# Performance work log

Measured on AMD Instinct MI355X. Metric: run time of the kernel, lower is better.

Reference implementation:

```python
import jax, jax.numpy as jnp
import numpy as np

IN_DIM, OUT_DIM, K, NUM = 512, 512, 3, 16
BATCH = 256


def setup_inputs() -> dict:
    key = jax.random.key(0)
    k1, k2 = jax.random.split(key, 2)
    x = jax.random.normal(k1, (BATCH, IN_DIM), dtype=jnp.float32)
    # uniform grid on [-1,1] extended by K knots each side (extend_grid)
    h = 2.0 / NUM
    g1d = jnp.arange(-K, NUM + K + 1, dtype=jnp.float32) * h - 1.0  # (NUM+1+2K,)
    grid = jnp.tile(g1d[None, :], (IN_DIM, 1))  # (in_dim, 24)
    coef = jax.random.normal(k2, (IN_DIM, OUT_DIM, NUM + K), dtype=jnp.float32) * 0.1
    scale_sp = jnp.ones((IN_DIM, OUT_DIM), jnp.float32) * (1.0 / np.sqrt(IN_DIM).astype(np.float32))
    mask = jnp.ones((IN_DIM, OUT_DIM), jnp.float32)
    return {"x": x, "grid": grid, "coef": coef, "scale_sp": scale_sp, "mask": mask}


def b_spline_basis(x, grid, k):
    # x: (B, I); grid: (I, G).  Cox-de Boor recursion, vectorized.
    xg = x[:, :, None]          # (B, I, 1)
    g = grid[None, :, :]        # (1, I, G)
    B = ((xg >= g[:, :, :-1]) & (xg < g[:, :, 1:])).astype(x.dtype)  # order-0
    for kk in range(1, k + 1):
        B = ((xg - g[:, :, :-(kk + 1)]) / (g[:, :, kk:-1] - g[:, :, :-(kk + 1)]) * B[:, :, :-1]
             + (g[:, :, kk + 1:] - xg) / (g[:, :, kk + 1:] - g[:, :, 1:-kk]) * B[:, :, 1:])
    return B  # (B, I, NUM + K)


def reference(x, grid, coef, scale_sp, mask):
    base = jax.nn.silu(x)                              # (B, I) base_fun branch
    Bmat = b_spline_basis(x, grid, K)                  # (B, I, NUM+K)
    y = jnp.einsum('big,iog->bio', Bmat, coef)         # coef2curve -> (B, I, O)
    y = (base[:, :, None] + scale_sp[None, :, :] * y) * mask[None, :, :]
    return jnp.sum(y, axis=1)                          # (B, O)
```

## Files before the change

### kernel.cpp

```cpp
#include <hip/hip_runtime.h>

#define IN_DIM   512
#define OUT_DIM  512
#define KDEG     3
#define BATCH    256
#define NB       19
#define NG       23
#define KAUG     20
#define KTOT     (IN_DIM * KAUG)

typedef short  bf16x8 __attribute__((ext_vector_type(8)));
typedef float  f32x4  __attribute__((ext_vector_type(4)));

__device__ __forceinline__ unsigned short f2bf(float f) {
    union { float f; unsigned int u; } v; v.f = f;
    unsigned int r = (v.u + 0x7FFF + ((v.u >> 16) & 1)) >> 16;
    return (unsigned short)r;
}

__global__ void build_A(const float* __restrict__ X,
                        const float* __restrict__ G,
                        unsigned short* __restrict__ A) {
    int t = blockIdx.x * blockDim.x + threadIdx.x;
    if (t >= BATCH * IN_DIM) return;
    int b = t / IN_DIM;
    int i = t - b * IN_DIM;

    float x = X[t];

    float gr[NG];
    const float* g = G + i * NG;
#pragma unroll
    for (int j = 0; j < NG; j++) gr[j] = g[j];

    float B[NG - 1];
#pragma unroll
    for (int j = 0; j < NG - 1; j++)
        B[j] = (x >= gr[j] && x < gr[j + 1]) ? 1.0f : 0.0f;

#pragma unroll
    for (int kk = 1; kk <= KDEG; kk++) {
#pragma unroll
        for (int j = 0; j < NG - 1 - kk; j++) {
            float d1 = gr[j + kk] - gr[j];
            float d2 = gr[j + kk + 1] - gr[j + 1];
            B[j] = (x - gr[j]) / d1 * B[j] +
                   (gr[j + kk + 1] - x) / d2 * B[j + 1];
        }
    }

    unsigned short v[KAUG];
#pragma unroll
    for (int j = 0; j < NB; j++) v[j] = f2bf(B[j]);
    v[NB] = f2bf(x / (1.0f + __expf(-x)));

    unsigned int* dst = (unsigned int*)(A + (size_t)b * KTOT + i * KAUG);
    const unsigned int* src = (const unsigned int*)v;
#pragma unroll
    for (int d = 0; d < KAUG / 2; d++) dst[d] = src[d];
}

#define BN     32
#define SPLITS 32
#define ICH    16
#define KCH    (ICH * KAUG)
#define LDS_K  (KCH + 8)

__global__ __launch_bounds__(512, 4) void gemm_fused(
        const unsigned short* __restrict__ A,
        const float* __restrict__ coef,
        const float* __restrict__ scale_sp,
        const float* __restrict__ mask,
        float* __restrict__ P) {
    __shared__ __align__(16) unsigned short Bs[BN * LDS_K];

    int tid = threadIdx.x;
    int o0 = blockIdx.x * BN;
    int i0 = blockIdx.z * ICH;
    int kbase = blockIdx.z * KCH;

    {
        int o  = tid & 31;
        int di = tid >> 5;
        int io = (i0 + di) * OUT_DIM + (o0 + o);
        float m  = mask[io];
        float sm = scale_sp[io] * m;
        const float* c = coef + (size_t)io * NB;

        __align__(8) unsigned short v[KAUG];
#pragma unroll
        for (int g = 0; g < NB; g++) v[g] = f2bf(c[g] * sm);
        v[NB] = f2bf(m);

        unsigned long long* dst =
            (unsigned long long*)((char*)Bs + (size_t)o * (LDS_K * 2) + di * (KAUG * 2));
        const unsigned long long* src = (const unsigned long long*)v;
#pragma unroll
        for (int d = 0; d < 5; d++) dst[d] = src[d];
    }
    __syncthreads();

    int lane = tid & 63;
    int w    = tid >> 6;
    int quad = lane >> 4;
    int lr   = lane & 15;

    f32x4 acc[2][2];
#pragma unroll
    for (int i = 0; i < 2; i++)
#pragma unroll
        for (int j = 0; j < 2; j++) acc[i][j] = (f32x4)0.0f;

    const unsigned short* a0 = A + (size_t)(w * 32 + lr)      * KTOT + kbase + quad * 8;
    const unsigned short* a1 = A + (size_t)(w * 32 + 16 + lr) * KTOT + kbase + quad * 8;
    const unsigned short* b0 = &Bs[(size_t)lr        * LDS_K + quad * 8];
    const unsigned short* b1 = &Bs[(size_t)(16 + lr) * LDS_K + quad * 8];

#pragma unroll
    for (int kk = 0; kk < KCH; kk += 32) {
        bf16x8 af0 = *(const bf16x8*)(a0 + kk);
        bf16x8 af1 = *(const bf16x8*)(a1 + kk);
        bf16x8 bf0 = *(const bf16x8*)(b0 + kk);
        bf16x8 bf1 = *(const bf16x8*)(b1 + kk);
        acc[0][0] = __builtin_amdgcn_mfma_f32_16x16x32_bf16(af0, bf0, acc[0][0], 0, 0, 0);
        acc[0][1] = __builtin_amdgcn_mfma_f32_16x16x32_bf16(af0, bf1, acc[0][1], 0, 0, 0);
        acc[1][0] = __builtin_amdgcn_mfma_f32_16x16x32_bf16(af1, bf0, acc[1][0], 0, 0, 0);
        acc[1][1] = __builtin_amdgcn_mfma_f32_16x16x32_bf16(af1, bf1, acc[1][1], 0, 0, 0);
    }

    float* Pz = P + (size_t)blockIdx.z * BATCH * OUT_DIM;
#pragma unroll
    for (int mt = 0; mt < 2; mt++) {
#pragma unroll
        for (int nt = 0; nt < 2; nt++) {
            int col = o0 + nt * 16 + lr;
            int rb  = w * 32 + mt * 16 + quad * 4;
#pragma unroll
            for (int r = 0; r < 4; r++)
                Pz[(size_t)(rb + r) * OUT_DIM + col] = acc[mt][nt][r];
        }
    }
}

__global__ __launch_bounds__(256) void reduce_out(const float* __restrict__ P,
                                                  float* __restrict__ out) {
    int e4 = blockIdx.x * blockDim.x + threadIdx.x;
    f32x4 s = (f32x4)0.0f;
#pragma unroll
    for (int z = 0; z < SPLITS; z++) {
        f32x4 v = *(const f32x4*)(P + (size_t)z * BATCH * OUT_DIM + e4 * 4);
        s += v;
    }
    *(f32x4*)((float*)out + (size_t)e4 * 4) = s;
}

extern "C" void kernel_launch(void* const* d_in, const int* in_sizes, int n_in,
                              void* d_out, int out_size, void* d_ws, size_t ws_size,
                              hipStream_t stream) {
    const float* x        = (const float*)d_in[0];
    const float* grid     = (const float*)d_in[1];
    const float* coef     = (const float*)d_in[2];
    const float* scale_sp = (const float*)d_in[3];
    const float* mask     = (const float*)d_in[4];
    float* out = (float*)d_out;

    unsigned short* A = (unsigned short*)d_ws;
    float* P = (float*)((char*)d_ws + (size_t)BATCH * KTOT * 2);

    build_A<<<dim3((BATCH * IN_DIM + 255) / 256), dim3(256), 0, stream>>>(x, grid, A);

    gemm_fused<<<dim3(OUT_DIM / BN, 1, SPLITS), dim3(512), 0, stream>>>(
        A, coef, scale_sp, mask, P);

    reduce_out<<<dim3(BATCH * OUT_DIM / 4 / 256), dim3(256), 0, stream>>>(P, out);
}
```

Baseline: 99.22 us.

## Pre-swizzle A and B into MFMA fragment layout, coalesce coef loads, retile GEMM

build_A now writes the spline basis matrix directly in MFMA fragment order through an LDS tile, so each lane reads a contiguous 16-byte fragment. The GEMM kernel stages coef through LDS with coalesced vector loads before scaling and converting it into fragment-ordered B, replacing the old strided per-thread coef reads. Tiles change to 128x64 with 256 threads and 2x4 MFMA accumulators per wave. The cost is more barriers in the B-build loop, and each coef tile is now rebuilt by two y-blocks.

```diff
diff --git a/kernel.cpp b/kernel.cpp
--- a/kernel.cpp
+++ b/kernel.cpp
@@ -8,6 +8,7 @@
 #define NG       23
 #define KAUG     20
 #define KTOT     (IN_DIM * KAUG)
+#define NKB_TOT  (KTOT / 32)
 
 typedef short  bf16x8 __attribute__((ext_vector_type(8)));
 typedef float  f32x4  __attribute__((ext_vector_type(4)));
@@ -18,126 +19,155 @@
     return (unsigned short)r;
 }
 
-__global__ void build_A(const float* __restrict__ X,
-                        const float* __restrict__ G,
-                        unsigned short* __restrict__ A) {
-    int t = blockIdx.x * blockDim.x + threadIdx.x;
-    if (t >= BATCH * IN_DIM) return;
-    int b = t / IN_DIM;
-    int i = t - b * IN_DIM;
-
-    float x = X[t];
-
-    float gr[NG];
-    const float* g = G + i * NG;
-#pragma unroll
-    for (int j = 0; j < NG; j++) gr[j] = g[j];
-
-    float B[NG - 1];
-#pragma unroll
-    for (int j = 0; j < NG - 1; j++)
-        B[j] = (x >= gr[j] && x < gr[j + 1]) ? 1.0f : 0.0f;
-
-#pragma unroll
-    for (int kk = 1; kk <= KDEG; kk++) {
-#pragma unroll
-        for (int j = 0; j < NG - 1 - kk; j++) {
-            float d1 = gr[j + kk] - gr[j];
-            float d2 = gr[j + kk + 1] - gr[j + 1];
-            B[j] = (x - gr[j]) / d1 * B[j] +
-                   (gr[j + kk + 1] - x) / d2 * B[j + 1];
-        }
-    }
-
-    unsigned short v[KAUG];
-#pragma unroll
-    for (int j = 0; j < NB; j++) v[j] = f2bf(B[j]);
-    v[NB] = f2bf(x / (1.0f + __expf(-x)));
-
-    unsigned int* dst = (unsigned int*)(A + (size_t)b * KTOT + i * KAUG);
-    const unsigned int* src = (const unsigned int*)v;
-#pragma unroll
-    for (int d = 0; d < KAUG / 2; d++) dst[d] = src[d];
-}
-
-#define BN     32
+
+__global__ __launch_bounds__(256) void build_A_frag(const float* __restrict__ X,
+                                                    const float* __restrict__ G,
+                                                    unsigned short* __restrict__ Af) {
+    __shared__ __align__(16) unsigned short tile[32 * KAUG * 16];
+
+    int t     = threadIdx.x;
+    int i0    = blockIdx.x * 32;
+    int m_blk = blockIdx.y;
+    int lr    = t & 15;
+    int b     = m_blk * 16 + lr;
+
+#pragma unroll
+    for (int r = 0; r < 2; r++) {
+        int il = (t >> 4) + (r << 4);
+        int i  = i0 + il;
+        float x = X[b * IN_DIM + i];
+
+        float gr[NG];
+        const float* g = G + i * NG;
+#pragma unroll
+        for (int j = 0; j < NG; j++) gr[j] = g[j];
+
+        float B[NG - 1];
+#pragma unroll
+        for (int j = 0; j < NG - 1; j++)
+            B[j] = (x >= gr[j] && x < gr[j + 1]) ? 1.0f : 0.0f;
+
+#pragma unroll
+        for (int kk = 1; kk <= KDEG; kk++) {
+#pragma unroll
+            for (int j = 0; j < NG - 1 - kk; j++) {
+                float d1 = gr[j + kk] - gr[j];
+                float d2 = gr[j + kk + 1] - gr[j + 1];
+                B[j] = (x - gr[j]) / d1 * B[j] +
+                       (gr[j + kk + 1] - x) / d2 * B[j + 1];
+            }
+        }
+
+        unsigned short v[KAUG];
+#pragma unroll
+        for (int j = 0; j < NB; j++) v[j] = f2bf(B[j]);
+        v[NB] = f2bf(x / (1.0f + __expf(-x)));
+
+#pragma unroll
+        for (int gidx = 0; gidx < KAUG; gidx++) {
+            int kl = il * KAUG + gidx;
+            tile[((kl >> 5) * 64 + ((kl & 31) >> 3) * 16 + lr) * 8 + (kl & 7)] = v[gidx];
+        }
+    }
+    __syncthreads();
+
+    const f32x4* src = (const f32x4*)tile;
+    f32x4* dst = (f32x4*)(Af + ((size_t)m_blk * NKB_TOT + blockIdx.x * 20) * 512);
+#pragma unroll
+    for (int r = 0; r < 5; r++) dst[t + r * 256] = src[t + r * 256];
+}
+
+#define BN     64
+#define BM     128
 #define SPLITS 32
 #define ICH    16
-#define KCH    (ICH * KAUG)
-#define LDS_K  (KCH + 8)
-
-__global__ __launch_bounds__(512, 4) void gemm_fused(
-        const unsigned short* __restrict__ A,
+#define NKB    10
+
+__global__ __launch_bounds__(256, 3) void gemm_fused(
+        const unsigned short* __restrict__ Af,
         const float* __restrict__ coef,
         const float* __restrict__ scale_sp,
         const float* __restrict__ mask,
         float* __restrict__ P) {
-    __shared__ __align__(16) unsigned short Bs[BN * LDS_K];
-
-    int tid = threadIdx.x;
+    __shared__ __align__(16) unsigned short Bf[4 * NKB * 512];
+    __shared__ __align__(16) float raw[2 * 64 * NB];
+
+    int t  = threadIdx.x;
     int o0 = blockIdx.x * BN;
-    int i0 = blockIdx.z * ICH;
-    int kbase = blockIdx.z * KCH;
-
-    {
-        int o  = tid & 31;
-        int di = tid >> 5;
-        int io = (i0 + di) * OUT_DIM + (o0 + o);
-        float m  = mask[io];
-        float sm = scale_sp[io] * m;
-        const float* c = coef + (size_t)io * NB;
-
-        __align__(8) unsigned short v[KAUG];
-#pragma unroll
-        for (int g = 0; g < NB; g++) v[g] = f2bf(c[g] * sm);
-        v[NB] = f2bf(m);
-
-        unsigned long long* dst =
-            (unsigned long long*)((char*)Bs + (size_t)o * (LDS_K * 2) + di * (KAUG * 2));
-        const unsigned long long* src = (const unsigned long long*)v;
-#pragma unroll
-        for (int d = 0; d < 5; d++) dst[d] = src[d];
-    }
-    __syncthreads();
-
-    int lane = tid & 63;
-    int w    = tid >> 6;
+    int y  = blockIdx.y;
+    int z  = blockIdx.z;
+    int i0 = z * ICH;
+
+    for (int c = 0; c < 8; c++) {
+        int ib = 2 * c;
+#pragma unroll
+        for (int seg = 0; seg < 2; seg++) {
+            const f32x4* gs = (const f32x4*)(coef +
+                ((size_t)(i0 + ib + seg) * OUT_DIM + o0) * NB);
+            f32x4* rs = (f32x4*)&raw[seg * 64 * NB];
+            for (int idx = t; idx < 304; idx += 256) rs[idx] = gs[idx];
+        }
+        __syncthreads();
+
+        if (t < 128) {
+            int seg   = t >> 6;
+            int o_loc = t & 63;
+            int i_loc = ib + seg;
+            int io = (i0 + i_loc) * OUT_DIM + (o0 + o_loc);
+            float m  = mask[io];
+            float sm = scale_sp[io] * m;
+            const float* cr = &raw[seg * 64 * NB + o_loc * NB];
+            int o_blk = o_loc >> 4;
+            int lro   = o_loc & 15;
+            int kb0   = i_loc * KAUG;
+#pragma unroll
+            for (int g = 0; g < KAUG; g++) {
+                float val = (g < NB) ? cr[g] * sm : m;
+                int kl = kb0 + g;
+                Bf[((o_blk * NKB + (kl >> 5)) * 64 + ((kl & 31) >> 3) * 16 + lro) * 8
+                   + (kl & 7)] = f2bf(val);
+            }
+        }
+        __syncthreads();
+    }
+
+    int lane = t & 63;
+    int w    = t >> 6;
     int quad = lane >> 4;
     int lr   = lane & 15;
 
-    f32x4 acc[2][2];
+    f32x4 acc[2][4];
 #pragma unroll
     for (int i = 0; i < 2; i++)
 #pragma unroll
-        for (int j = 0; j < 2; j++) acc[i][j] = (f32x4)0.0f;
-
-    const unsigned short* a0 = A + (size_t)(w * 32 + lr)      * KTOT + kbase + quad * 8;
-    const unsigned short* a1 = A + (size_t)(w * 32 + 16 + lr) * KTOT + kbase + quad * 8;
-    const unsigned short* b0 = &Bs[(size_t)lr        * LDS_K + quad * 8];
-    const unsigned short* b1 = &Bs[(size_t)(16 + lr) * LDS_K + quad * 8];
-
-#pragma unroll
-    for (int kk = 0; kk < KCH; kk += 32) {
-        bf16x8 af0 = *(const bf16x8*)(a0 + kk);
-        bf16x8 af1 = *(const bf16x8*)(a1 + kk);
-        bf16x8 bf0 = *(const bf16x8*)(b0 + kk);
-        bf16x8 bf1 = *(const bf16x8*)(b1 + kk);
-        acc[0][0] = __builtin_amdgcn_mfma_f32_16x16x32_bf16(af0, bf0, acc[0][0], 0, 0, 0);
-        acc[0][1] = __builtin_amdgcn_mfma_f32_16x16x32_bf16(af0, bf1, acc[0][1], 0, 0, 0);
-        acc[1][0] = __builtin_amdgcn_mfma_f32_16x16x32_bf16(af1, bf0, acc[1][0], 0, 0, 0);
-        acc[1][1] = __builtin_amdgcn_mfma_f32_16x16x32_bf16(af1, bf1, acc[1][1], 0, 0, 0);
-    }
-
-    float* Pz = P + (size_t)blockIdx.z * BATCH * OUT_DIM;
+        for (int j = 0; j < 4; j++) acc[i][j] = (f32x4)0.0f;
+
+    int mb0 = y * 8 + w * 2;
+    const unsigned short* A0 = Af + (((size_t)(mb0 + 0) * NKB_TOT + z * NKB) * 64 + lane) * 8;
+    const unsigned short* A1 = Af + (((size_t)(mb0 + 1) * NKB_TOT + z * NKB) * 64 + lane) * 8;
+
+#pragma unroll
+    for (int kb = 0; kb < NKB; kb++) {
+        bf16x8 a0 = *(const bf16x8*)(A0 + (size_t)kb * 512);
+        bf16x8 a1 = *(const bf16x8*)(A1 + (size_t)kb * 512);
+#pragma unroll
+        for (int nt = 0; nt < 4; nt++) {
+            bf16x8 bfr = *(const bf16x8*)&Bf[((nt * NKB + kb) * 64 + lane) * 8];
+            acc[0][nt] = __builtin_amdgcn_mfma_f32_16x16x32_bf16(a0, bfr, acc[0][nt], 0, 0, 0);
+            acc[1][nt] = __builtin_amdgcn_mfma_f32_16x16x32_bf16(a1, bfr, acc[1][nt], 0, 0, 0);
+        }
+    }
+
+    float* Pz = P + (size_t)z * BATCH * OUT_DIM;
 #pragma unroll
     for (int mt = 0; mt < 2; mt++) {
-#pragma unroll
-        for (int nt = 0; nt < 2; nt++) {
+        int bb = (mb0 + mt) * 16 + quad * 4;
+#pragma unroll
+        for (int nt = 0; nt < 4; nt++) {
             int col = o0 + nt * 16 + lr;
-            int rb  = w * 32 + mt * 16 + quad * 4;
 #pragma unroll
             for (int r = 0; r < 4; r++)
-                Pz[(size_t)(rb + r) * OUT_DIM + col] = acc[mt][nt][r];
+                Pz[(size_t)(bb + r) * OUT_DIM + col] = acc[mt][nt][r];
         }
     }
 }
@@ -147,8 +177,8 @@
     int e4 = blockIdx.x * blockDim.x + threadIdx.x;
     f32x4 s = (f32x4)0.0f;
 #pragma unroll
-    for (int z = 0; z < SPLITS; z++) {
-        f32x4 v = *(const f32x4*)(P + (size_t)z * BATCH * OUT_DIM + e4 * 4);
+    for (int zz = 0; zz < SPLITS; zz++) {
+        f32x4 v = *(const f32x4*)(P + (size_t)zz * BATCH * OUT_DIM + e4 * 4);
         s += v;
     }
     *(f32x4*)((float*)out + (size_t)e4 * 4) = s;
@@ -164,13 +194,13 @@
     const float* mask     = (const float*)d_in[4];
     float* out = (float*)d_out;
 
-    unsigned short* A = (unsigned short*)d_ws;
+    unsigned short* Af = (unsigned short*)d_ws;
     float* P = (float*)((char*)d_ws + (size_t)BATCH * KTOT * 2);
 
-    build_A<<<dim3((BATCH * IN_DIM + 255) / 256), dim3(256), 0, stream>>>(x, grid, A);
-
-    gemm_fused<<<dim3(OUT_DIM / BN, 1, SPLITS), dim3(512), 0, stream>>>(
-        A, coef, scale_sp, mask, P);
+    build_A_frag<<<dim3(16, 16), dim3(256), 0, stream>>>(x, grid, Af);
+
+    gemm_fused<<<dim3(OUT_DIM / BN, BATCH / BM, SPLITS), dim3(256), 0, stream>>>(
+        Af, coef, scale_sp, mask, P);
 
     reduce_out<<<dim3(BATCH * OUT_DIM / 4 / 256), dim3(256), 0, stream>>>(P, out);
 }
```

New measurement: 108.3 us. +9.2%, slower.
